# Kernel optimization log

Hardware: AMD Instinct MI355X
Metric: run time of the kernel (lower is better)

## Reference

```python
import jax, jax.numpy as jnp
import numpy as np

N = 100000   # nodes
E = 500000   # edges
D = 128      # node_hidden_size
ED = 128     # edge_emb_dim
L = 8        # n_message_passes
H = 4        # num_heads
V = 8192     # node_vocab_size
G = 64       # num_graphs
A = 100      # num_actions
NFLOW = 8
NPOS = 64


def setup_inputs() -> dict:
    key = jax.random.key(0)
    ks = jax.random.split(key, 24)
    rn = lambda k, shape, s: jax.random.normal(k, shape, jnp.float32) * s
    inp = {}
    # graph tensors
    inp['x'] = jax.random.randint(ks[0], (N,), 0, V)
    inp['node_type'] = jax.random.randint(ks[1], (N,), 0, 2)
    inp['batch'] = jnp.sort(jax.random.randint(ks[2], (N,), 0, G))
    inp['edge_index'] = jax.random.randint(ks[3], (2, E), 0, N)
    inp['flow'] = jax.random.randint(ks[4], (E,), 0, NFLOW)
    inp['position'] = jax.random.randint(ks[5], (E,), 0, NPOS)
    inp['block'] = jax.random.randint(ks[6], (N,), 0, 4096)
    inp['num_graphs'] = G
    # parameters
    sd = 1.0 / np.sqrt(D)
    se = 1.0 / np.sqrt(ED)
    inp['emb_table'] = rn(ks[7], (V, D), 1.0)
    inp['flow_emb'] = rn(ks[8], (NFLOW, ED), 1.0)
    inp['pos_emb'] = rn(ks[9], (NPOS, ED), 1.0)
    inp['blk_emb'] = rn(ks[10], (2, ED), 1.0)
    inp['Wq'] = rn(ks[11], (L, D, D), sd)
    inp['Wk'] = rn(ks[12], (L, D, D), sd)
    inp['Wv'] = rn(ks[13], (L, D, D), sd)
    inp['Wek'] = rn(ks[14], (L, ED, D), se)
    inp['Wev'] = rn(ks[15], (L, ED, D), se)
    inp['Wo'] = rn(ks[16], (L, D, D), sd)
    inp['Weu'] = rn(ks[17], (L, 2 * D + ED, ED), 1.0 / np.sqrt(2 * D + ED))
    inp['QW1'] = rn(ks[18], (D + ED, D), 1.0 / np.sqrt(D + ED))
    inp['Qb1'] = jnp.zeros((D,), jnp.float32)
    inp['QW2'] = rn(ks[19], (D, A), sd)
    inp['Qb2'] = jnp.zeros((A,), jnp.float32)
    return inp


def _forward(x, node_type, batch, edge_index, flow, position, block, num_graphs,
             emb_table, flow_emb, pos_emb, blk_emb,
             Wq, Wk, Wv, Wek, Wev, Wo, Weu, QW1, Qb1, QW2, Qb2):
    src, dst = edge_index[0], edge_index[1]
    feat = emb_table[x]                                        # [N, D]
    # EdgeEncoding: flow-type + position embeddings + block-crossing indicator
    crossing = (block[src] != block[dst]).astype(jnp.int32)
    e = flow_emb[flow] + pos_emb[position] + blk_emb[crossing]  # [E, ED]

    Nn, Dd = feat.shape
    dh = Dd // H
    scale = 1.0 / np.sqrt(dh)
    n_layers = Wq.shape[0]
    for l in range(n_layers):
        q = (feat @ Wq[l]).reshape(Nn, H, dh)
        k = (feat @ Wk[l]).reshape(Nn, H, dh)
        v = (feat @ Wv[l]).reshape(Nn, H, dh)
        ek = (e @ Wek[l]).reshape(-1, H, dh)
        ev = (e @ Wev[l]).reshape(-1, H, dh)
        # per-edge attention logits, softmax over edges sharing a dst node
        scores = jnp.sum(q[dst] * (k[src] + ek), axis=-1) * scale  # [E, H]
        m = jax.lax.stop_gradient(
            jax.ops.segment_max(scores, dst, num_segments=Nn))
        ex = jnp.exp(scores - m[dst])
        den = jax.ops.segment_sum(ex, dst, num_segments=Nn)
        alpha = ex / (den[dst] + 1e-16)                            # [E, H]
        msg = alpha[..., None] * (v[src] + ev)                     # [E, H, dh]
        agg = jax.ops.segment_sum(msg, dst, num_segments=Nn).reshape(Nn, Dd)
        feat_new = jax.nn.relu(feat + agg @ Wo[l])
        e = jax.nn.relu(e + jnp.concatenate([feat[src], feat[dst], e], axis=-1) @ Weu[l])
        feat = feat_new

    # scatter_mean over instruction nodes (type == 0) per graph
    maskf = (node_type == 0).astype(feat.dtype)
    ncnt = jax.ops.segment_sum(maskf, batch, num_segments=num_graphs)
    gagg = jax.ops.segment_sum(feat * maskf[:, None], batch, num_segments=num_graphs)
    gagg = gagg / jnp.maximum(ncnt, 1.0)[:, None]
    # scatter_mean of edge features per graph (edge's graph = graph of its src node)
    eb = batch[src]
    ecnt = jax.ops.segment_sum(jnp.ones((e.shape[0],), e.dtype), eb, num_segments=num_graphs)
    eagg = jax.ops.segment_sum(e, eb, num_segments=num_graphs)
    eagg = eagg / jnp.maximum(ecnt, 1.0)[:, None]

    ga = jnp.concatenate([gagg, eagg], axis=-1)                    # [G, D+ED]
    h = jax.nn.relu(ga @ QW1 + Qb1)
    logits = h @ QW2 + Qb2
    return jax.nn.log_softmax(logits, axis=-1)


def reference(x, node_type, batch, edge_index, flow, position, block, num_graphs,
              emb_table, flow_emb, pos_emb, blk_emb,
              Wq, Wk, Wv, Wek, Wev, Wo, Weu, QW1, Qb1, QW2, Qb2):
    return _forward(x, node_type, batch, edge_index, flow, position, block,
                    int(num_graphs), emb_table, flow_emb, pos_emb, blk_emb,
                    Wq, Wk, Wv, Wek, Wev, Wo, Weu, QW1, Qb1, QW2, Qb2)
```

## Files before the change

### kernel.cpp

```cpp
#include <hip/hip_runtime.h>
#include <stdint.h>

#define NN 100000
#define NE 500000
#define DD 128
#define NL 8
#define NG 64
#define NA 100
#define DET_PAIRS 65536

typedef unsigned short u16;
typedef unsigned int u32;
typedef __attribute__((ext_vector_type(8))) short short8;
typedef __attribute__((ext_vector_type(4))) float f32x4;

union U4 { uint4 v; u16 s[8]; };

__device__ __forceinline__ float b2f(u16 u){ union{u32 i; float f;} x; x.i=((u32)u)<<16; return x.f; }
__device__ __forceinline__ u16 f2b(float f){ union{float f; u32 i;} x; x.f=f; u32 b=x.i; b += 0x7fffu + ((b>>16)&1u); return (u16)(b>>16); }

__global__ void zero_k(int* __restrict__ p, int n){
  int i = blockIdx.x*256 + threadIdx.x;
  if (i < n) p[i] = 0;
}
__global__ void diag_k(u16* __restrict__ out, int n, float val){
  int i = blockIdx.x*256 + threadIdx.x;
  if (i < n) out[i] = f2b(val);
}

__global__ void detect_k(const u16* __restrict__ raw, int* __restrict__ flags){
  int i = blockIdx.x*256 + threadIdx.x;
  int ok = 0;
  if (i < DET_PAIRS){
    u16 v = raw[2*i];
    int e = (v>>7)&0xFF;
    ok = ((e >= 107 && e <= 147) || ((v & 0x7FFFu) == 0)) ? 1 : 0;
  }
  unsigned long long b = __ballot(ok);
  if ((threadIdx.x & 63) == 0) atomicAdd(&flags[2], (int)__popcll(b));
}
__global__ void flagset_k(int* __restrict__ flags){
  if (threadIdx.x==0) flags[0] = (flags[2] < DET_PAIRS/2) ? 1 : 0;
}
__global__ void tobf16_k(const void* __restrict__ in, u16* __restrict__ out, int n,
                         const int* __restrict__ flags){
  int i = blockIdx.x*256 + threadIdx.x;
  if (i >= n) return;
  if (flags[0]) out[i] = f2b(((const float*)in)[i]);
  else          out[i] = ((const u16*)in)[i];
}
__global__ void convT_k(const void* __restrict__ in, u16* __restrict__ out, int L, int K, int Nn,
                        const int* __restrict__ flags){
  int id = blockIdx.x*256 + threadIdx.x;
  int tot = L*K*Nn;
  if (id >= tot) return;
  int l = id/(K*Nn); int r = id - l*K*Nn;
  int k = r/Nn; int n = r - k*Nn;
  u16 v;
  if (flags[0]) v = f2b(((const float*)in)[id]);
  else          v = ((const u16*)in)[id];
  out[(size_t)l*K*Nn + (size_t)n*K + k] = v;
}

__global__ void featinit_k(const int* __restrict__ x, const u16* __restrict__ emb, u16* __restrict__ feat){
  int id = blockIdx.x*256 + threadIdx.x;
  if (id >= NN*16) return;
  int row = id>>4, c8 = (id&15)*8;
  int g = x[row];
  *(uint4*)(feat + (size_t)row*DD + c8) = *(const uint4*)(emb + (size_t)g*DD + c8);
}

__global__ void count_k(const int* __restrict__ dst, int* __restrict__ cnt){
  int e = blockIdx.x*256 + threadIdx.x;
  if (e < NE) atomicAdd(&cnt[dst[e]], 1);
}
__global__ void scan1_k(const int* __restrict__ cnt, int* __restrict__ excl, int* __restrict__ bsum, int n){
  __shared__ int sh[256];
  int t = threadIdx.x, g = blockIdx.x*256 + t;
  int v = (g<n) ? cnt[g] : 0;
  sh[t] = v; __syncthreads();
  for (int d=1; d<256; d<<=1){
    int xv = (t>=d) ? sh[t-d] : 0;
    __syncthreads();
    sh[t] += xv;
    __syncthreads();
  }
  if (g<n) excl[g] = sh[t]-v;
  if (t==255) bsum[blockIdx.x] = sh[255];
}
__global__ void scan2_k(int* __restrict__ bsum, int nb){
  if (threadIdx.x==0 && blockIdx.x==0){
    int a=0;
    for (int i=0;i<nb;i++){ int x=bsum[i]; bsum[i]=a; a+=x; }
  }
}
__global__ void scan3_k(const int* __restrict__ excl, const int* __restrict__ bsum,
                        int* __restrict__ offs, int* __restrict__ cursor, int n, int total){
  int g = blockIdx.x*256 + threadIdx.x;
  if (g < n){ int o = excl[g] + bsum[g>>8]; offs[g]=o; cursor[g]=o; }
  if (g==0) offs[n] = total;
}
__global__ void fill_k(const int* __restrict__ dst, int* __restrict__ cursor, int* __restrict__ perm){
  int e = blockIdx.x*256 + threadIdx.x;
  if (e < NE){ int p = atomicAdd(&cursor[dst[e]], 1); perm[p] = e; }
}
__global__ void make_sorted_k(const int* __restrict__ perm, const int* __restrict__ src,
                              const int* __restrict__ dst, int* __restrict__ srcs, int* __restrict__ dsts){
  int i = blockIdx.x*256 + threadIdx.x;
  if (i < NE){ int ed = perm[i]; srcs[i] = src[ed]; dsts[i] = dst[ed]; }
}

__global__ void edgeinit_k(const int* __restrict__ perm, const int* __restrict__ flow,
                           const int* __restrict__ pos, const int* __restrict__ blk,
                           const int* __restrict__ srcs, const int* __restrict__ dsts,
                           const int* __restrict__ batch,
                           const u16* __restrict__ flow_emb, const u16* __restrict__ pos_emb,
                           const u16* __restrict__ blk_emb,
                           u16* __restrict__ e, int* __restrict__ ebgs){
  int id = blockIdx.x*256 + threadIdx.x;
  if (id >= NE*16) return;
  int i = id>>4, c8 = (id&15)*8;
  int ed = perm[i];
  int s = srcs[i], d = dsts[i];
  int cross = (blk[s] != blk[d]) ? 1 : 0;
  U4 a,b,c,o;
  a.v = *(const uint4*)(flow_emb + (size_t)flow[ed]*DD + c8);
  b.v = *(const uint4*)(pos_emb  + (size_t)pos[ed]*DD + c8);
  c.v = *(const uint4*)(blk_emb  + (size_t)cross*DD + c8);
  #pragma unroll
  for (int j=0;j<8;j++) o.s[j] = f2b(b2f(a.s[j]) + b2f(b.s[j]) + b2f(c.s[j]));
  *(uint4*)(e + (size_t)i*DD + c8) = o.v;
  if ((id&15)==0) ebgs[i] = batch[s];
}

__global__ __launch_bounds__(256,4) void gemm_k(
    const u16* A0, const int* __restrict__ i0,
    const u16* A1, const int* __restrict__ i1,
    const u16* A2, const int* __restrict__ i2, int nchunks,
    const u16* __restrict__ Bt, int Ktot,
    const u16* res, int do_relu,
    u16* C, int M)
{
  __shared__ u16 As[128*128];
  int t = threadIdx.x;
  int mbase = blockIdx.x*128;
  int lane = t & 63, w = t>>6;
  int wrow = (w>>1)*64, wcol = (w&1)*64;
  int rl_w = t>>4, gw = t&15;
  int l15 = lane & 15, quad = lane>>4;
  f32x4 acc[4][4];
  #pragma unroll
  for (int mi=0;mi<4;mi++)
    #pragma unroll
    for (int ni=0;ni<4;ni++){ acc[mi][ni][0]=0.f; acc[mi][ni][1]=0.f; acc[mi][ni][2]=0.f; acc[mi][ni][3]=0.f; }

  for (int c=0; c<nchunks; c++){
    const u16* A = (c==0)?A0:((c==1)?A1:A2);
    const int* idx = (c==0)?i0:((c==1)?i1:i2);
    if (c > 0) __syncthreads();
    #pragma unroll
    for (int i=0;i<8;i++){
      int gm = mbase + rl_w + 16*i;
      uint4 av = make_uint4(0u,0u,0u,0u);
      if (gm < M){
        size_t grow = idx ? (size_t)idx[gm] : (size_t)gm;
        av = *(const uint4*)(A + grow*DD + gw*8);
      }
      *(uint4*)(As + (size_t)(i*256 + rl_w*16 + (gw ^ rl_w))*8) = av;
    }
    __syncthreads();
    #pragma unroll
    for (int kk=0;kk<4;kk++){
      int kg = kk*4 + quad;
      short8 af[4], bfr[4];
      #pragma unroll
      for (int mi=0;mi<4;mi++)
        af[mi] = *(const short8*)(As + (size_t)(((wrow>>4)+mi)*256 + l15*16 + (kg ^ l15))*8);
      #pragma unroll
      for (int ni=0;ni<4;ni++)
        bfr[ni] = *(const short8*)(Bt + (size_t)(wcol + ni*16 + l15)*Ktot + c*128 + kg*8);
      #pragma unroll
      for (int mi=0;mi<4;mi++)
        #pragma unroll
        for (int ni=0;ni<4;ni++)
          acc[mi][ni] = __builtin_amdgcn_mfma_f32_16x16x32_bf16(af[mi], bfr[ni], acc[mi][ni], 0, 0, 0);
    }
  }

  __syncthreads();
  #pragma unroll
  for (int mi=0;mi<4;mi++){
    #pragma unroll
    for (int r4=0;r4<4;r4++){
      int row = wrow + mi*16 + quad*4 + r4;
      #pragma unroll
      for (int ni=0;ni<4;ni++){
        int col = wcol + ni*16 + l15;
        As[row*128 + ((((col>>3) ^ (row&15))<<3)) + (col&7)] = f2b(acc[mi][ni][r4]);
      }
    }
  }
  __syncthreads();
  #pragma unroll
  for (int i=0;i<8;i++){
    int row = rl_w + 16*i;
    int gm = mbase + row;
    if (gm >= M) continue;
    U4 av; av.v = *(const uint4*)(As + row*128 + ((gw ^ (row&15))<<3));
    float vals[8];
    #pragma unroll
    for (int j=0;j<8;j++) vals[j] = b2f(av.s[j]);
    if (res){
      U4 rv; rv.v = *(const uint4*)(res + (size_t)gm*DD + gw*8);
      #pragma unroll
      for (int j=0;j<8;j++) vals[j] += b2f(rv.s[j]);
    }
    U4 ov;
    #pragma unroll
    for (int j=0;j<8;j++){
      float v = vals[j];
      if (do_relu && v < 0.f) v = 0.f;
      ov.s[j] = f2b(v);
    }
    *(uint4*)(C + (size_t)gm*DD + gw*8) = ov.v;
  }
}

__global__ __launch_bounds__(256,4) void scores_fused_k(
    const u16* __restrict__ E, const u16* __restrict__ WekT,
    const u16* __restrict__ q, const u16* __restrict__ k,
    const int* __restrict__ srcs, const int* __restrict__ dsts,
    float* __restrict__ sc)
{
  __shared__ u16 As[128*128];
  int t = threadIdx.x;
  int ebase = blockIdx.x*128;
  int lane = t & 63, w = t>>6;
  int wrow = (w>>1)*64, wcol = (w&1)*64;
  int rl_w = t>>4, gw = t&15;
  int l15 = lane & 15, quad = lane>>4;
  #pragma unroll
  for (int i=0;i<8;i++){
    int gm = ebase + rl_w + 16*i;
    uint4 av = make_uint4(0u,0u,0u,0u);
    if (gm < NE) av = *(const uint4*)(E + (size_t)gm*DD + gw*8);
    *(uint4*)(As + (size_t)(i*256 + rl_w*16 + (gw ^ rl_w))*8) = av;
  }
  __syncthreads();
  f32x4 acc[4][4];
  #pragma unroll
  for (int mi=0;mi<4;mi++)
    #pragma unroll
    for (int ni=0;ni<4;ni++){ acc[mi][ni][0]=0.f; acc[mi][ni][1]=0.f; acc[mi][ni][2]=0.f; acc[mi][ni][3]=0.f; }
  #pragma unroll
  for (int kk=0;kk<4;kk++){
    int kg = kk*4 + quad;
    short8 af[4], bfr[4];
    #pragma unroll
    for (int mi=0;mi<4;mi++)
      af[mi] = *(const short8*)(As + (size_t)(((wrow>>4)+mi)*256 + l15*16 + (kg ^ l15))*8);
    #pragma unroll
    for (int ni=0;ni<4;ni++)
      bfr[ni] = *(const short8*)(WekT + (size_t)(wcol + ni*16 + l15)*DD + kg*8);
    #pragma unroll
    for (int mi=0;mi<4;mi++)
      #pragma unroll
      for (int ni=0;ni<4;ni++)
        acc[mi][ni] = __builtin_amdgcn_mfma_f32_16x16x32_bf16(af[mi], bfr[ni], acc[mi][ni], 0, 0, 0);
  }
  __syncthreads();
  #pragma unroll
  for (int mi=0;mi<4;mi++){
    #pragma unroll
    for (int r4=0;r4<4;r4++){
      int row = wrow + mi*16 + quad*4 + r4;
      #pragma unroll
      for (int ni=0;ni<4;ni++){
        int col = wcol + ni*16 + l15;
        As[row*128 + ((((col>>3) ^ (row&15))<<3)) + (col&7)] = f2b(acc[mi][ni][r4]);
      }
    }
  }
  __syncthreads();
  const float scale = 0.17677669529663689f;
  for (int pid = t; pid < 512; pid += 256){
    int le = pid>>2, h = pid&3;
    int e = ebase + le;
    if (e >= NE) continue;
    int s = srcs[e], d = dsts[e];
    float dot = 0.f;
    #pragma unroll
    for (int j4=0;j4<4;j4++){
      int off = h*32 + j4*8;
      U4 qv, kv, ev;
      qv.v = *(const uint4*)(q + (size_t)d*DD + off);
      kv.v = *(const uint4*)(k + (size_t)s*DD + off);
      ev.v = *(const uint4*)(As + le*128 + ((((h*4+j4) ^ (le&15))<<3)));
      #pragma unroll
      for (int j=0;j<8;j++) dot += b2f(qv.s[j]) * (b2f(kv.s[j]) + b2f(ev.s[j]));
    }
    sc[(size_t)e*4 + h] = dot * scale;
  }
}

__global__ __launch_bounds__(256,2) void nodeagg_k(
    const float* __restrict__ sc, const u16* __restrict__ v,
    const u16* __restrict__ E, const int* __restrict__ srcs,
    const int* __restrict__ offs, const u16* __restrict__ WevL,
    u16* __restrict__ agg)
{
  __shared__ float sh[16*4*129];
  int t = threadIdx.x;
  int node = blockIdx.x*16 + (t>>4);
  int sub = t & 15, h = sub>>2, p4 = sub&3;
  float uh[32];
  #pragma unroll
  for (int j=0;j<32;j++) uh[j]=0.f;
  float accv[8] = {0.f,0.f,0.f,0.f,0.f,0.f,0.f,0.f};
  int beg = 0, end = 0;
  if (node < NN){ beg = offs[node]; end = offs[node+1]; }
  float m = -1e30f, den = 0.f;
  for (int i=beg;i<end;i++){
    float s = sc[(size_t)i*4 + h];
    float mn = fmaxf(m, s);
    den = den*__expf(m-mn) + __expf(s-mn);
    m = mn;
  }
  float inv = 1.0f/(den + 1e-16f);
  int offv = h*32 + p4*8;
  for (int i=beg;i<end;i++){
    float a = __expf(sc[(size_t)i*4 + h] - m)*inv;
    U4 vv; vv.v = *(const uint4*)(v + (size_t)srcs[i]*DD + offv);
    #pragma unroll
    for (int j=0;j<8;j++) accv[j] += a*b2f(vv.s[j]);
    const u16* er = E + (size_t)i*DD + p4*32;
    #pragma unroll
    for (int qq=0;qq<4;qq++){
      U4 ee; ee.v = *(const uint4*)(er + qq*8);
      #pragma unroll
      for (int j=0;j<8;j++) uh[qq*8+j] += a*b2f(ee.s[j]);
    }
  }
  int base = ((t>>4)*4 + h)*129;
  #pragma unroll
  for (int j=0;j<32;j++) sh[base + p4*32 + j] = uh[j];
  __syncthreads();
  if (node >= NN) return;
  float o8[8];
  #pragma unroll
  for (int j=0;j<8;j++) o8[j] = accv[j];
  for (int kk=0;kk<128;kk+=4){
    float u0 = sh[base+kk], u1 = sh[base+kk+1], u2 = sh[base+kk+2], u3 = sh[base+kk+3];
    U4 w0,w1,w2,w3;
    w0.v = *(const uint4*)(WevL + (size_t)kk*DD + offv);
    w1.v = *(const uint4*)(WevL + (size_t)(kk+1)*DD + offv);
    w2.v = *(const uint4*)(WevL + (size_t)(kk+2)*DD + offv);
    w3.v = *(const uint4*)(WevL + (size_t)(kk+3)*DD + offv);
    #pragma unroll
    for (int j=0;j<8;j++)
      o8[j] += u0*b2f(w0.s[j]) + u1*b2f(w1.s[j]) + u2*b2f(w2.s[j]) + u3*b2f(w3.s[j]);
  }
  U4 o;
  #pragma unroll
  for (int j=0;j<8;j++) o.s[j] = f2b(o8[j]);
  *(uint4*)(agg + (size_t)node*DD + offv) = o.v;
}

__global__ void hist_k(const int* __restrict__ gid, const int* __restrict__ mask, int n,
                       int* __restrict__ hist){
  __shared__ int lh[NG];
  int t = threadIdx.x;
  if (t < NG) lh[t]=0;
  __syncthreads();
  int i = blockIdx.x*256 + t;
  if (i < n && (!mask || mask[i]==0)) atomicAdd(&lh[gid[i]], 1);
  __syncthreads();
  if (t < NG && lh[t]) atomicAdd(&hist[t], lh[t]);
}
__global__ void scan64_k(const int* __restrict__ hist, int* __restrict__ base, int* __restrict__ cur){
  if (threadIdx.x==0){
    int a=0;
    for (int g=0; g<NG; g++){ base[g]=a; cur[g]=a; a+=hist[g]; }
    base[NG]=a;
  }
}
__global__ void fillperm_k(const int* __restrict__ gid, const int* __restrict__ mask, int n,
                           int* __restrict__ cur, int* __restrict__ operm){
  __shared__ int lh[NG];
  __shared__ int lb[NG];
  int t = threadIdx.x;
  if (t < NG) lh[t]=0;
  __syncthreads();
  int i = blockIdx.x*256 + t;
  int g=-1, r=0;
  if (i < n && (!mask || mask[i]==0)){ g = gid[i]; r = atomicAdd(&lh[g], 1); }
  __syncthreads();
  if (t < NG && lh[t]) lb[t] = atomicAdd(&cur[t], lh[t]);
  __syncthreads();
  if (g >= 0) operm[lb[g] + r] = i;
}
__global__ __launch_bounds__(256,4) void poolsum_k(
    const u16* __restrict__ feat, const int* __restrict__ operm,
    const int* __restrict__ base, int chunks, float* __restrict__ outsum)
{
  __shared__ float sh[16*128];
  int g = blockIdx.x / chunks, c = blockIdx.x % chunks;
  int beg = base[g], end = base[g+1];
  int len = end - beg;
  int cb = beg + (int)(((long long)len*c)/chunks);
  int ce = beg + (int)(((long long)len*(c+1))/chunks);
  int t = threadIdx.x, grp = t>>4, sub = t&15;
  float acc[8] = {0.f,0.f,0.f,0.f,0.f,0.f,0.f,0.f};
  for (int i = cb+grp; i < ce; i += 16){
    int r = operm[i];
    U4 fv; fv.v = *(const uint4*)(feat + (size_t)r*DD + sub*8);
    #pragma unroll
    for (int j=0;j<8;j++) acc[j] += b2f(fv.s[j]);
  }
  #pragma unroll
  for (int j=0;j<8;j++) sh[grp*128 + sub*8 + j] = acc[j];
  __syncthreads();
  if (t < 128){
    float s = 0.f;
    #pragma unroll
    for (int r=0;r<16;r++) s += sh[r*128 + t];
    if (s != 0.f) atomicAdd(&outsum[g*DD + t], s);
  }
}

__global__ void ganorm_k(const float* __restrict__ gsum, const int* __restrict__ ncnt,
                         const float* __restrict__ esum, const int* __restrict__ ecnt,
                         float* __restrict__ ga){
  int id = blockIdx.x*256 + threadIdx.x;
  if (id >= NG*256) return;
  int g = id>>8, c = id&255;
  float v;
  if (c < 128) v = gsum[g*DD + c] / fmaxf((float)ncnt[g], 1.f);
  else         v = esum[g*DD + (c-128)] / fmaxf((float)ecnt[g], 1.f);
  ga[(size_t)g*256 + c] = v;
}

__global__ void mlp1_k(const float* __restrict__ ga, const u16* __restrict__ QW1,
                       const u16* __restrict__ Qb1, float* __restrict__ h){
  int o = blockIdx.x*256 + threadIdx.x;
  if (o >= NG*DD) return;
  int g = o>>7, j = o&127;
  float s = b2f(Qb1[j]);
  #pragma unroll 4
  for (int kq=0;kq<256;kq++) s += ga[(size_t)g*256 + kq] * b2f(QW1[(size_t)kq*DD + j]);
  h[o] = fmaxf(s, 0.f);
}

__global__ __launch_bounds__(128) void mlp2_k(const float* __restrict__ h, const u16* __restrict__ QW2,
                       const u16* __restrict__ Qb2, void* __restrict__ out, const int* __restrict__ flags){
  __shared__ float lsh[NA];
  __shared__ float red[128];
  int g = blockIdx.x, t = threadIdx.x;
  float s = -1e30f;
  if (t < NA){
    float acc = b2f(Qb2[t]);
    #pragma unroll 4
    for (int kq=0;kq<DD;kq++) acc += h[(size_t)g*DD + kq] * b2f(QW2[(size_t)kq*NA + t]);
    lsh[t] = acc; s = acc;
  }
  red[t] = s; __syncthreads();
  for (int d=64; d>0; d>>=1){ if (t<d) red[t] = fmaxf(red[t], red[t+d]); __syncthreads(); }
  float m = red[0]; __syncthreads();
  float ex = (t < NA) ? __expf(lsh[t]-m) : 0.f;
  red[t] = ex; __syncthreads();
  for (int d=64; d>0; d>>=1){ if (t<d) red[t] += red[t+d]; __syncthreads(); }
  float lse = m + __logf(red[0]);
  if (t < NA){
    float r = lsh[t]-lse;
    if (flags[0]) ((float*)out)[(size_t)g*NA + t] = r;
    else          ((u16*)out)[(size_t)g*NA + t]  = f2b(r);
  }
}

extern "C" void kernel_launch(void* const* d_in, const int* in_sizes, int n_in,
                              void* d_out, int out_size, void* d_ws, size_t ws_size,
                              hipStream_t stream) {
  (void)in_sizes; (void)n_in;
  const int* x      = (const int*)d_in[0];
  const int* ntype  = (const int*)d_in[1];
  const int* batch  = (const int*)d_in[2];
  const int* eidx   = (const int*)d_in[3];
  const int* src    = eidx;
  const int* dstp   = eidx + NE;
  const int* flow   = (const int*)d_in[4];
  const int* pos    = (const int*)d_in[5];
  const int* blk    = (const int*)d_in[6];

  char* p = (char*)d_ws;
  auto alloc = [&](size_t bytes)->char* {
    char* r = p; p += (bytes + 255) & ~(size_t)255; return r;
  };
  u16* embB  = (u16*)alloc((size_t)8192*DD*2);
  u16* flowB = (u16*)alloc(8*DD*2);
  u16* posB  = (u16*)alloc(64*DD*2);
  u16* blkB  = (u16*)alloc(2*DD*2);
  const size_t WSZb = (size_t)NL*DD*DD*2;
  u16* WevB = (u16*)alloc(WSZb);
  u16* QW1B = (u16*)alloc((size_t)256*DD*2);
  u16* Qb1B = (u16*)alloc(DD*2);
  u16* QW2B = (u16*)alloc((size_t)DD*NA*2);
  u16* Qb2B = (u16*)alloc(NA*2);
  u16* WqT  = (u16*)alloc(WSZb);
  u16* WkT  = (u16*)alloc(WSZb);
  u16* WvT  = (u16*)alloc(WSZb);
  u16* WekT = (u16*)alloc(WSZb);
  u16* WoT  = (u16*)alloc(WSZb);
  u16* WeuT = (u16*)alloc((size_t)NL*DD*384*2);
  const size_t NB = (size_t)NN*DD*2;
  u16* A  = (u16*)alloc(NB);
  u16* QB = (u16*)alloc(NB);
  u16* KB = (u16*)alloc(NB);
  u16* SCRATCH = (u16*)alloc(NB);
  const size_t EB = (size_t)NE*DD*2;
  u16* E = (u16*)alloc(EB);
  float* scores = (float*)alloc((size_t)NE*4*4);
  int* srcs   = (int*)alloc((size_t)NE*4);
  int* dsts   = (int*)alloc((size_t)NE*4);
  int* ebgs   = (int*)alloc((size_t)NE*4);
  int* offs   = (int*)alloc((size_t)(NN+1)*4);
  float* gsum = (float*)alloc((size_t)NG*DD*4);
  float* esum = (float*)alloc((size_t)NG*DD*4);
  float* ga = (float*)alloc((size_t)NG*256*4);
  float* h  = (float*)alloc((size_t)NG*DD*4);
  int* flags = (int*)alloc(16);

  char* q = (char*)SCRATCH;
  auto suballoc = [&](size_t bytes)->char* {
    char* r = q; q += (bytes + 255) & ~(size_t)255; return r;
  };
  int* perm   = (int*)suballoc((size_t)NE*4);
  int* cnt    = (int*)suballoc((size_t)NN*4);
  int* excl   = (int*)suballoc((size_t)NN*4);
  int* bsum   = (int*)suballoc(1024*4);
  int* cursor = (int*)suballoc((size_t)NN*4);
  int* eperm  = (int*)suballoc((size_t)NE*4);
  int* nperm  = (int*)suballoc((size_t)NN*4);
  int* ehist  = (int*)suballoc(NG*4);
  int* ebase  = (int*)suballoc((NG+1)*4);
  int* ecur   = (int*)suballoc(NG*4);
  int* nhist  = (int*)suballoc(NG*4);
  int* nbase  = (int*)suballoc((NG+1)*4);
  int* ncur   = (int*)suballoc(NG*4);

  size_t needed = (size_t)(p - (char*)d_ws);
  if (needed > ws_size){
    diag_k<<<(out_size+255)/256,256,0,stream>>>((u16*)d_out, out_size, (float)(ws_size>>20));
    return;
  }

  zero_k<<<1,256,0,stream>>>(flags, 4);
  detect_k<<<(DET_PAIRS+255)/256,256,0,stream>>>((const u16*)d_in[8], flags);
  flagset_k<<<1,64,0,stream>>>(flags);
  auto conv = [&](int idx, u16* dst, int n){
    tobf16_k<<<(n+255)/256,256,0,stream>>>(d_in[idx], dst, n, flags);
  };
  auto convT = [&](int idx, u16* dst, int L, int K, int Nc){
    int n = L*K*Nc;
    convT_k<<<(n+255)/256,256,0,stream>>>(d_in[idx], dst, L, K, Nc, flags);
  };
  conv(8,  embB,  8192*DD);
  conv(9,  flowB, 8*DD);
  conv(10, posB,  64*DD);
  conv(11, blkB,  2*DD);
  convT(12, WqT,  NL, DD, DD);
  convT(13, WkT,  NL, DD, DD);
  convT(14, WvT,  NL, DD, DD);
  convT(15, WekT, NL, DD, DD);
  conv(16, WevB, NL*DD*DD);
  convT(17, WoT,  NL, DD, DD);
  convT(18, WeuT, NL, 384, DD);
  conv(19, QW1B, 256*DD);
  conv(20, Qb1B, DD);
  conv(21, QW2B, DD*NA);
  conv(22, Qb2B, NA);

  zero_k<<<(NN+255)/256,256,0,stream>>>(cnt, NN);
  count_k<<<(NE+255)/256,256,0,stream>>>(dstp, cnt);
  int nb = (NN+255)/256;
  scan1_k<<<nb,256,0,stream>>>(cnt, excl, bsum, NN);
  scan2_k<<<1,64,0,stream>>>(bsum, nb);
  scan3_k<<<nb,256,0,stream>>>(excl, bsum, offs, cursor, NN, NE);
  fill_k<<<(NE+255)/256,256,0,stream>>>(dstp, cursor, perm);
  make_sorted_k<<<(NE+255)/256,256,0,stream>>>(perm, src, dstp, srcs, dsts);
  featinit_k<<<(NN*16+255)/256,256,0,stream>>>(x, embB, A);
  edgeinit_k<<<(NE*16+255)/256,256,0,stream>>>(perm, flow, pos, blk, srcs, dsts, batch,
                                               flowB, posB, blkB, E, ebgs);

  dim3 gN((NN+127)/128), gE((NE+127)/128);
  for (int l=0; l<NL; l++){
    const u16* wq  = WqT  + (size_t)l*DD*DD;
    const u16* wk  = WkT  + (size_t)l*DD*DD;
    const u16* wv  = WvT  + (size_t)l*DD*DD;
    const u16* wek = WekT + (size_t)l*DD*DD;
    const u16* wo  = WoT  + (size_t)l*DD*DD;
    const u16* wevL= WevB + (size_t)l*DD*DD;
    const u16* weu = WeuT + (size_t)l*DD*384;

    gemm_k<<<gN,256,0,stream>>>(A,nullptr,nullptr,nullptr,nullptr,nullptr,1, wq,128, nullptr,0, QB, NN);
    gemm_k<<<gN,256,0,stream>>>(A,nullptr,nullptr,nullptr,nullptr,nullptr,1, wk,128, nullptr,0, KB, NN);
    scores_fused_k<<<gE,256,0,stream>>>(E, wek, QB, KB, srcs, dsts, scores);
    gemm_k<<<gN,256,0,stream>>>(A,nullptr,nullptr,nullptr,nullptr,nullptr,1, wv,128, nullptr,0, KB, NN);
    nodeagg_k<<<(NN+15)/16,256,0,stream>>>(scores, KB, E, srcs, offs, wevL, QB);
    gemm_k<<<gE,256,0,stream>>>(A,srcs, A,dsts, E,nullptr, 3, weu,384, E,1, E, NE);
    gemm_k<<<gN,256,0,stream>>>(QB,nullptr,nullptr,nullptr,nullptr,nullptr,1, wo,128, A,1, A, NN);
  }

  zero_k<<<1,256,0,stream>>>(ehist, NG);
  zero_k<<<1,256,0,stream>>>(nhist, NG);
  zero_k<<<(NG*DD+255)/256,256,0,stream>>>((int*)gsum, NG*DD);
  zero_k<<<(NG*DD+255)/256,256,0,stream>>>((int*)esum, NG*DD);
  hist_k<<<(NE+255)/256,256,0,stream>>>(ebgs, nullptr, NE, ehist);
  hist_k<<<(NN+255)/256,256,0,stream>>>(batch, ntype, NN, nhist);
  scan64_k<<<1,64,0,stream>>>(ehist, ebase, ecur);
  scan64_k<<<1,64,0,stream>>>(nhist, nbase, ncur);
  fillperm_k<<<(NE+255)/256,256,0,stream>>>(ebgs, nullptr, NE, ecur, eperm);
  fillperm_k<<<(NN+255)/256,256,0,stream>>>(batch, ntype, NN, ncur, nperm);
  const int ECH = 16, NCH = 4;
  poolsum_k<<<NG*ECH,256,0,stream>>>(E, eperm, ebase, ECH, esum);
  poolsum_k<<<NG*NCH,256,0,stream>>>(A, nperm, nbase, NCH, gsum);
  ganorm_k<<<(NG*256+255)/256,256,0,stream>>>(gsum, nhist, esum, ehist, ga);
  mlp1_k<<<(NG*DD+255)/256,256,0,stream>>>(ga, QW1B, Qb1B, h);
  mlp2_k<<<NG,128,0,stream>>>(h, QW2B, Qb2B, d_out, flags);
}
```

Measured before the change: 4.681 ms.

## Reuse LDS-resident residual in edge GEMM and coalesce nodeagg edge loads

In the edge-update GEMM, the residual E is now read from the last K-chunk still held in shared memory instead of being reloaded from global memory, with residual add and ReLU applied in registers before the store. The nodeagg kernel is rearranged so each thread handles an 8-column slice across all four heads, reading one float4 of scores and one 16-byte E chunk per edge instead of four strided chunks. This reduces global traffic in two kernels that run every layer. The cost is four softmax states and a 32-float accumulator per thread in nodeagg, plus a correctness dependence on the last chunk being E.

```diff
diff --git a/kernel.cpp b/kernel.cpp
--- a/kernel.cpp
+++ b/kernel.cpp
@@ -138,7 +138,7 @@
     const u16* A1, const int* __restrict__ i1,
     const u16* A2, const int* __restrict__ i2, int nchunks,
     const u16* __restrict__ Bt, int Ktot,
-    const u16* res, int do_relu,
+    const u16* res, int do_relu, int res_lds,
     u16* C, int M)
 {
   __shared__ u16 As[128*128];
@@ -187,6 +187,23 @@
     }
   }
 
+  if (res_lds){
+    #pragma unroll
+    for (int mi=0;mi<4;mi++){
+      #pragma unroll
+      for (int r4=0;r4<4;r4++){
+        int row = wrow + mi*16 + quad*4 + r4;
+        #pragma unroll
+        for (int ni=0;ni<4;ni++){
+          int col = wcol + ni*16 + l15;
+          float r = b2f(As[(row>>4)*2048 + (row&15)*128 + (((col>>3) ^ (row&15))<<3) + (col&7)]);
+          float vv = acc[mi][ni][r4] + r;
+          if (do_relu && vv < 0.f) vv = 0.f;
+          acc[mi][ni][r4] = vv;
+        }
+      }
+    }
+  }
   __syncthreads();
   #pragma unroll
   for (int mi=0;mi<4;mi++){
@@ -207,6 +224,10 @@
     int gm = mbase + row;
     if (gm >= M) continue;
     U4 av; av.v = *(const uint4*)(As + row*128 + ((gw ^ (row&15))<<3));
+    if (res_lds){
+      *(uint4*)(C + (size_t)gm*DD + gw*8) = av.v;
+      continue;
+    }
     float vals[8];
     #pragma unroll
     for (int j=0;j<8;j++) vals[j] = b2f(av.s[j]);
@@ -311,51 +332,66 @@
 {
   __shared__ float sh[16*4*129];
   int t = threadIdx.x;
-  int node = blockIdx.x*16 + (t>>4);
-  int sub = t & 15, h = sub>>2, p4 = sub&3;
-  float uh[32];
-  #pragma unroll
-  for (int j=0;j<32;j++) uh[j]=0.f;
-  float accv[8] = {0.f,0.f,0.f,0.f,0.f,0.f,0.f,0.f};
+  int n16 = t>>4;
+  int node = blockIdx.x*16 + n16;
+  int sub = t & 15;
+  int hown = sub>>2;
+  int offc = sub*8;
   int beg = 0, end = 0;
   if (node < NN){ beg = offs[node]; end = offs[node+1]; }
-  float m = -1e30f, den = 0.f;
+  float m[4] = {-1e30f,-1e30f,-1e30f,-1e30f};
+  float den[4] = {0.f,0.f,0.f,0.f};
   for (int i=beg;i<end;i++){
-    float s = sc[(size_t)i*4 + h];
-    float mn = fmaxf(m, s);
-    den = den*__expf(m-mn) + __expf(s-mn);
-    m = mn;
-  }
-  float inv = 1.0f/(den + 1e-16f);
-  int offv = h*32 + p4*8;
+    float4 s4 = *(const float4*)(sc + (size_t)i*4);
+    float ss[4] = {s4.x, s4.y, s4.z, s4.w};
+    #pragma unroll
+    for (int h=0;h<4;h++){
+      float mn = fmaxf(m[h], ss[h]);
+      den[h] = den[h]*__expf(m[h]-mn) + __expf(ss[h]-mn);
+      m[h] = mn;
+    }
+  }
+  float inv[4];
+  #pragma unroll
+  for (int h=0;h<4;h++) inv[h] = 1.0f/(den[h] + 1e-16f);
+  float uh[4][8];
+  #pragma unroll
+  for (int h=0;h<4;h++)
+    #pragma unroll
+    for (int j=0;j<8;j++) uh[h][j]=0.f;
+  float accv[8] = {0.f,0.f,0.f,0.f,0.f,0.f,0.f,0.f};
   for (int i=beg;i<end;i++){
-    float a = __expf(sc[(size_t)i*4 + h] - m)*inv;
-    U4 vv; vv.v = *(const uint4*)(v + (size_t)srcs[i]*DD + offv);
-    #pragma unroll
-    for (int j=0;j<8;j++) accv[j] += a*b2f(vv.s[j]);
-    const u16* er = E + (size_t)i*DD + p4*32;
-    #pragma unroll
-    for (int qq=0;qq<4;qq++){
-      U4 ee; ee.v = *(const uint4*)(er + qq*8);
-      #pragma unroll
-      for (int j=0;j<8;j++) uh[qq*8+j] += a*b2f(ee.s[j]);
-    }
-  }
-  int base = ((t>>4)*4 + h)*129;
-  #pragma unroll
-  for (int j=0;j<32;j++) sh[base + p4*32 + j] = uh[j];
+    float4 s4 = *(const float4*)(sc + (size_t)i*4);
+    float al[4] = { __expf(s4.x-m[0])*inv[0], __expf(s4.y-m[1])*inv[1],
+                    __expf(s4.z-m[2])*inv[2], __expf(s4.w-m[3])*inv[3] };
+    U4 ee; ee.v = *(const uint4*)(E + (size_t)i*DD + offc);
+    #pragma unroll
+    for (int j=0;j<8;j++){
+      float ev = b2f(ee.s[j]);
+      #pragma unroll
+      for (int h=0;h<4;h++) uh[h][j] += al[h]*ev;
+    }
+    U4 vv; vv.v = *(const uint4*)(v + (size_t)srcs[i]*DD + offc);
+    #pragma unroll
+    for (int j=0;j<8;j++) accv[j] += al[hown]*b2f(vv.s[j]);
+  }
+  #pragma unroll
+  for (int h=0;h<4;h++)
+    #pragma unroll
+    for (int j=0;j<8;j++) sh[(n16*4 + h)*129 + offc + j] = uh[h][j];
   __syncthreads();
   if (node >= NN) return;
   float o8[8];
   #pragma unroll
   for (int j=0;j<8;j++) o8[j] = accv[j];
+  int base = (n16*4 + hown)*129;
   for (int kk=0;kk<128;kk+=4){
     float u0 = sh[base+kk], u1 = sh[base+kk+1], u2 = sh[base+kk+2], u3 = sh[base+kk+3];
     U4 w0,w1,w2,w3;
-    w0.v = *(const uint4*)(WevL + (size_t)kk*DD + offv);
-    w1.v = *(const uint4*)(WevL + (size_t)(kk+1)*DD + offv);
-    w2.v = *(const uint4*)(WevL + (size_t)(kk+2)*DD + offv);
-    w3.v = *(const uint4*)(WevL + (size_t)(kk+3)*DD + offv);
+    w0.v = *(const uint4*)(WevL + (size_t)kk*DD + offc);
+    w1.v = *(const uint4*)(WevL + (size_t)(kk+1)*DD + offc);
+    w2.v = *(const uint4*)(WevL + (size_t)(kk+2)*DD + offc);
+    w3.v = *(const uint4*)(WevL + (size_t)(kk+3)*DD + offc);
     #pragma unroll
     for (int j=0;j<8;j++)
       o8[j] += u0*b2f(w0.s[j]) + u1*b2f(w1.s[j]) + u2*b2f(w2.s[j]) + u3*b2f(w3.s[j]);
@@ -363,7 +399,7 @@
   U4 o;
   #pragma unroll
   for (int j=0;j<8;j++) o.s[j] = f2b(o8[j]);
-  *(uint4*)(agg + (size_t)node*DD + offv) = o.v;
+  *(uint4*)(agg + (size_t)node*DD + offc) = o.v;
 }
 
 __global__ void hist_k(const int* __restrict__ gid, const int* __restrict__ mask, int n,
@@ -601,13 +637,13 @@
     const u16* wevL= WevB + (size_t)l*DD*DD;
     const u16* weu = WeuT + (size_t)l*DD*384;
 
-    gemm_k<<<gN,256,0,stream>>>(A,nullptr,nullptr,nullptr,nullptr,nullptr,1, wq,128, nullptr,0, QB, NN);
-    gemm_k<<<gN,256,0,stream>>>(A,nullptr,nullptr,nullptr,nullptr,nullptr,1, wk,128, nullptr,0, KB, NN);
+    gemm_k<<<gN,256,0,stream>>>(A,nullptr,nullptr,nullptr,nullptr,nullptr,1, wq,128, nullptr,0,0, QB, NN);
+    gemm_k<<<gN,256,0,stream>>>(A,nullptr,nullptr,nullptr,nullptr,nullptr,1, wk,128, nullptr,0,0, KB, NN);
     scores_fused_k<<<gE,256,0,stream>>>(E, wek, QB, KB, srcs, dsts, scores);
-    gemm_k<<<gN,256,0,stream>>>(A,nullptr,nullptr,nullptr,nullptr,nullptr,1, wv,128, nullptr,0, KB, NN);
+    gemm_k<<<gN,256,0,stream>>>(A,nullptr,nullptr,nullptr,nullptr,nullptr,1, wv,128, nullptr,0,0, KB, NN);
     nodeagg_k<<<(NN+15)/16,256,0,stream>>>(scores, KB, E, srcs, offs, wevL, QB);
-    gemm_k<<<gE,256,0,stream>>>(A,srcs, A,dsts, E,nullptr, 3, weu,384, E,1, E, NE);
-    gemm_k<<<gN,256,0,stream>>>(QB,nullptr,nullptr,nullptr,nullptr,nullptr,1, wo,128, A,1, A, NN);
+    gemm_k<<<gE,256,0,stream>>>(A,srcs, A,dsts, E,nullptr, 3, weu,384, nullptr,1,1, E, NE);
+    gemm_k<<<gN,256,0,stream>>>(QB,nullptr,nullptr,nullptr,nullptr,nullptr,1, wo,128, A,1,0, A, NN);
   }
 
   zero_k<<<1,256,0,stream>>>(ehist, NG);
```

New measurement: 4.544 ms. -2.9%, faster.
